# Kernel optimization log

Measured on AMD Instinct MI355X. Metric: run time of the kernel, lower is better.

Reference implementation:

```python
import jax, jax.numpy as jnp
import numpy as np

STU_NUM, ITEM_NUM, CONC_NUM, EMB_DIM, BATCH = 20000, 8000, 128, 32, 128


def setup_inputs() -> dict:
    key = jax.random.key(0)
    ks = jax.random.split(key, 12)
    # 1-based student ids, as in the original (forward does stu - 1)
    stu_list = jax.random.randint(ks[0], (BATCH,), 1, STU_NUM + 1, dtype=jnp.int32)
    stu_emb = jax.random.normal(ks[1], (STU_NUM, EMB_DIM), jnp.float32)
    item_emb = jax.random.normal(ks[2], (ITEM_NUM, EMB_DIM), jnp.float32)
    disc = jax.random.normal(ks[3], (ITEM_NUM, 1), jnp.float32)
    # binary Q-matrix (item x concept), float as in Q.float()
    Q = (jax.random.uniform(ks[4], (ITEM_NUM, CONC_NUM)) < 0.3).astype(jnp.float32)
    # emb2conc: Linear(emb_dim, conc_num) + sigmoid
    w1 = jax.random.normal(ks[5], (CONC_NUM, EMB_DIM), jnp.float32) / np.sqrt(EMB_DIM)
    b1 = jax.random.normal(ks[6], (CONC_NUM,), jnp.float32) * 0.1
    # pred_layer: Linear(conc_num, 1) + sigmoid
    wp = jax.random.normal(ks[7], (1, CONC_NUM), jnp.float32) / np.sqrt(CONC_NUM)
    bp = jax.random.normal(ks[8], (1,), jnp.float32) * 0.1
    gw_stu = jax.random.normal(ks[9], (STU_NUM, 1), jnp.float32)
    gw_Q = jax.random.normal(ks[10], (CONC_NUM, 1), jnp.float32)
    # guess_adju_layer2: Linear(1,1) + sigmoid
    w2 = jax.random.normal(ks[11], (1, 1), jnp.float32)
    b2 = jnp.zeros((1,), jnp.float32)
    return {"stu_list": stu_list, "stu_emb": stu_emb, "item_emb": item_emb,
            "disc": disc, "Q": Q, "w1": w1, "b1": b1, "wp": wp, "bp": bp,
            "gw_stu": gw_stu, "gw_Q": gw_Q, "w2": w2, "b2": b2}


def reference(stu_list, stu_emb, item_emb, disc, Q, w1, b1, wp, bp, gw_stu, gw_Q, w2, b2):
    idx = stu_list - 1                                        # 1-based -> 0-based
    stu_conc = jax.nn.sigmoid(stu_emb[idx] @ w1.T + b1)       # [B, C]
    item_conc = jax.nn.sigmoid(item_emb @ w1.T + b1)          # [I, C]
    # X = Q * (stu_emb_conc - item_emb_conc) * disc, batched over students
    X = Q[None, :, :] * (stu_conc[:, None, :] - item_conc[None, :, :]) * disc[None, :, :]  # [B, I, C]
    P = jax.nn.sigmoid(jnp.einsum('bic,c->bi', X, wp[0]) + bp[0])   # [B, I]
    Q_adju = (Q @ gw_Q)[:, 0]                                 # [I]
    g1 = jax.nn.sigmoid(gw_stu[idx] + Q_adju[None, :])        # [B,1]+[1,I] -> [B, I]
    g2 = jax.nn.sigmoid(g1 * w2[0, 0] + b2[0])                # Linear(1,1)+sigmoid
    return g2 + (1.0 - g2) * P                                # [B, I]
```

## Files before the change

### kernel.cpp

```cpp
#include <hip/hip_runtime.h>
#include <hip/hip_bf16.h>

#define STU  20000
#define ITEM 8000
#define CONC 128
#define EMB  32
#define BATCH 128

typedef short s16x8 __attribute__((ext_vector_type(8)));
typedef float f32x4 __attribute__((ext_vector_type(4)));

__device__ __forceinline__ float sigmoidf(float x) { return 1.f / (1.f + __expf(-x)); }

__global__ __launch_bounds__(256) void stu_kernel(
    const int* __restrict__ stu_list, const float* __restrict__ stu_emb,
    const float* __restrict__ w1, const float* __restrict__ b1,
    const float* __restrict__ gw_stu,
    __hip_bfloat16* __restrict__ scb_out,
    float* __restrict__ gs_out)
{
    int tid = blockIdx.x * 256 + threadIdx.x;
    int b = tid >> 7, c = tid & 127;
    int sid = stu_list[b] - 1;
    float d = b1[c];
    const float4* wrow = (const float4*)(w1 + c * EMB);
    const float4* erow = (const float4*)(stu_emb + (size_t)sid * EMB);
#pragma unroll
    for (int e4 = 0; e4 < EMB / 4; ++e4) {
        float4 w = wrow[e4], em = erow[e4];
        d += w.x * em.x + w.y * em.y + w.z * em.z + w.w * em.w;
    }
    scb_out[tid] = __float2bfloat16(sigmoidf(d) - 0.5f);
    if (c == 0) gs_out[b] = gw_stu[sid];
}

__global__ __launch_bounds__(256) void item_kernel(
    const float* __restrict__ item_emb, const float* __restrict__ Q,
    const float* __restrict__ w1, const float* __restrict__ b1,
    const float* __restrict__ wp, const float* __restrict__ gw_Q,
    __hip_bfloat16* __restrict__ qwb_out,
    float* __restrict__ t2_out,
    float* __restrict__ qa_out)
{
    const int wave = (blockIdx.x * 256 + threadIdx.x) >> 6;
    const int lane = threadIdx.x & 63;
    const int c0 = lane, c1 = lane + 64;

    float4 wa[8], wb[8];
    const float4* w0p = (const float4*)(w1 + c0 * EMB);
    const float4* w1p = (const float4*)(w1 + c1 * EMB);
#pragma unroll
    for (int j = 0; j < 8; ++j) { wa[j] = w0p[j]; wb[j] = w1p[j]; }
    const float b10 = b1[c0], b11 = b1[c1];
    const float wp0 = wp[c0], wp1 = wp[c1];
    const float gq0 = gw_Q[c0], gq1 = gw_Q[c1];

    for (int n = 0; n < 8; ++n) {
        const int i = wave * 8 + n;
        const float4* ep = (const float4*)(item_emb + (size_t)i * EMB);
        float d0 = b10, d1 = b11;
#pragma unroll
        for (int j = 0; j < 8; ++j) {
            float4 e = ep[j];
            d0 += wa[j].x * e.x + wa[j].y * e.y + wa[j].z * e.z + wa[j].w * e.w;
            d1 += wb[j].x * e.x + wb[j].y * e.y + wb[j].z * e.z + wb[j].w * e.w;
        }
        float ic0 = sigmoidf(d0), ic1 = sigmoidf(d1);
        float q0 = Q[(size_t)i * CONC + c0], q1 = Q[(size_t)i * CONC + c1];
        float u0 = q0 * wp0, u1 = q1 * wp1;
        qwb_out[(size_t)i * CONC + c0] = __float2bfloat16(u0);
        qwb_out[(size_t)i * CONC + c1] = __float2bfloat16(u1);
        float at = u0 * ic0 + u1 * ic1;
        float as = u0 + u1;
        float aq = q0 * gq0 + q1 * gq1;
#pragma unroll
        for (int off = 32; off; off >>= 1) {
            at += __shfl_xor(at, off);
            as += __shfl_xor(as, off);
            aq += __shfl_xor(aq, off);
        }
        if (lane == 0) { t2_out[i] = at - 0.5f * as; qa_out[i] = aq; }
    }
}

__global__ __launch_bounds__(256) void out_mfma(
    const __hip_bfloat16* __restrict__ qwb, const __hip_bfloat16* __restrict__ scb,
    const float* __restrict__ disc, const float* __restrict__ t2,
    const float* __restrict__ qa, const float* __restrict__ gs,
    const float* __restrict__ w2, const float* __restrict__ b2,
    const float* __restrict__ bpp,
    float* __restrict__ out)
{
    const int wid  = (blockIdx.x * 256 + threadIdx.x) >> 6;
    const int lane = threadIdx.x & 63;
    const int it = wid % 500, bt = wid / 500;
    const int i0 = it * 16, b0 = bt * 16;
    const int l15 = lane & 15, lk = lane >> 4;

    const s16x8* ap  = (const s16x8*)((const short*)scb + (b0 + l15) * CONC + lk * 8);
    const s16x8* bp8 = (const s16x8*)((const short*)qwb + (size_t)(i0 + l15) * CONC + lk * 8);

    f32x4 acc = {0.f, 0.f, 0.f, 0.f};
#pragma unroll
    for (int ks = 0; ks < 4; ++ks)
        acc = __builtin_amdgcn_mfma_f32_16x16x32_bf16(ap[ks * 4], bp8[ks * 4], acc, 0, 0, 0);

    const int i = i0 + l15;
    const float di = disc[i], ti = t2[i], qi = qa[i];
    const float W2 = w2[0], B2 = b2[0], BP = bpp[0];
#pragma unroll
    for (int r = 0; r < 4; ++r) {
        const int b = b0 + lk * 4 + r;
        float P  = sigmoidf(di * (acc[r] - ti) + BP);
        float g1 = sigmoidf(gs[b] + qi);
        float g2 = sigmoidf(fmaf(g1, W2, B2));
        out[(size_t)b * ITEM + i] = g2 + (1.f - g2) * P;
    }
}

extern "C" void kernel_launch(void* const* d_in, const int* in_sizes, int n_in,
                              void* d_out, int out_size, void* d_ws, size_t ws_size,
                              hipStream_t stream) {
    const int*   stu_list = (const int*)d_in[0];
    const float* stu_emb  = (const float*)d_in[1];
    const float* item_emb = (const float*)d_in[2];
    const float* disc     = (const float*)d_in[3];
    const float* Q        = (const float*)d_in[4];
    const float* w1       = (const float*)d_in[5];
    const float* b1       = (const float*)d_in[6];
    const float* wp       = (const float*)d_in[7];
    const float* bp       = (const float*)d_in[8];
    const float* gw_stu   = (const float*)d_in[9];
    const float* gw_Q     = (const float*)d_in[10];
    const float* w2       = (const float*)d_in[11];
    const float* b2       = (const float*)d_in[12];
    float* out = (float*)d_out;

    char* ws = (char*)d_ws;
    __hip_bfloat16* scb = (__hip_bfloat16*)ws;
    float* gs  = (float*)(ws + 32768);
    float* t2  = gs + BATCH;
    float* qa  = t2 + ITEM;
    __hip_bfloat16* qwb = (__hip_bfloat16*)(ws + 32768 + 4 * (BATCH + 2 * ITEM));

    stu_kernel<<<64, 256, 0, stream>>>(stu_list, stu_emb, w1, b1, gw_stu, scb, gs);
    item_kernel<<<250, 256, 0, stream>>>(item_emb, Q, w1, b1, wp, gw_Q, qwb, t2, qa);
    out_mfma<<<1000, 256, 0, stream>>>(qwb, scb, disc, t2, qa, gs, w2, b2, bp, out);
}
```

Before: 103.9 us.

## Fuse student, item and output stages into one MFMA kernel with LDS staging

Merges the three separate kernels into one, where each block recomputes the student concept matrix via bf16 MFMA in LDS, computes its 16 items' concept terms, and performs the output MFMA directly from shared memory. This removes two kernel launches and global workspace round trips. It adds redundant per-block student-projection work, higher LDS use that limits occupancy, and bf16 rounding of the embedding projections.

```diff
diff --git a/kernel.cpp b/kernel.cpp
--- a/kernel.cpp
+++ b/kernel.cpp
@@ -1,120 +1,157 @@
 #include <hip/hip_runtime.h>
 #include <hip/hip_bf16.h>
 
-#define STU  20000
 #define ITEM 8000
 #define CONC 128
 #define EMB  32
 #define BATCH 128
+#define NBLK 500
+#define IB   16
+#define SE_S 56
+#define SC_S 136
 
 typedef short s16x8 __attribute__((ext_vector_type(8)));
 typedef float f32x4 __attribute__((ext_vector_type(4)));
 
 __device__ __forceinline__ float sigmoidf(float x) { return 1.f / (1.f + __expf(-x)); }
-
-__global__ __launch_bounds__(256) void stu_kernel(
-    const int* __restrict__ stu_list, const float* __restrict__ stu_emb,
-    const float* __restrict__ w1, const float* __restrict__ b1,
-    const float* __restrict__ gw_stu,
-    __hip_bfloat16* __restrict__ scb_out,
-    float* __restrict__ gs_out)
-{
-    int tid = blockIdx.x * 256 + threadIdx.x;
-    int b = tid >> 7, c = tid & 127;
-    int sid = stu_list[b] - 1;
-    float d = b1[c];
-    const float4* wrow = (const float4*)(w1 + c * EMB);
-    const float4* erow = (const float4*)(stu_emb + (size_t)sid * EMB);
-#pragma unroll
-    for (int e4 = 0; e4 < EMB / 4; ++e4) {
-        float4 w = wrow[e4], em = erow[e4];
-        d += w.x * em.x + w.y * em.y + w.z * em.z + w.w * em.w;
-    }
-    scb_out[tid] = __float2bfloat16(sigmoidf(d) - 0.5f);
-    if (c == 0) gs_out[b] = gw_stu[sid];
+__device__ __forceinline__ short f2bf(float x) {
+    __hip_bfloat16 h = __float2bfloat16(x);
+    return *reinterpret_cast<short*>(&h);
+}
+__device__ __forceinline__ void cvt16(const float4* __restrict__ src, short* dst) {
+    float4 f0 = src[0], f1 = src[1], f2 = src[2], f3 = src[3];
+    s16x8 a, b;
+    a[0]=f2bf(f0.x); a[1]=f2bf(f0.y); a[2]=f2bf(f0.z); a[3]=f2bf(f0.w);
+    a[4]=f2bf(f1.x); a[5]=f2bf(f1.y); a[6]=f2bf(f1.z); a[7]=f2bf(f1.w);
+    b[0]=f2bf(f2.x); b[1]=f2bf(f2.y); b[2]=f2bf(f2.z); b[3]=f2bf(f2.w);
+    b[4]=f2bf(f3.x); b[5]=f2bf(f3.y); b[6]=f2bf(f3.z); b[7]=f2bf(f3.w);
+    *(s16x8*)dst = a;
+    *(s16x8*)(dst + 8) = b;
 }
 
-__global__ __launch_bounds__(256) void item_kernel(
-    const float* __restrict__ item_emb, const float* __restrict__ Q,
-    const float* __restrict__ w1, const float* __restrict__ b1,
-    const float* __restrict__ wp, const float* __restrict__ gw_Q,
-    __hip_bfloat16* __restrict__ qwb_out,
-    float* __restrict__ t2_out,
-    float* __restrict__ qa_out)
+__global__ __launch_bounds__(256) void fused_kernel(
+    const int* __restrict__ stu_list, const float* __restrict__ stu_emb,
+    const float* __restrict__ item_emb, const float* __restrict__ disc,
+    const float* __restrict__ Q, const float* __restrict__ w1,
+    const float* __restrict__ b1, const float* __restrict__ wp,
+    const float* __restrict__ bp_, const float* __restrict__ gw_stu,
+    const float* __restrict__ gw_Q, const float* __restrict__ w2,
+    const float* __restrict__ b2, float* __restrict__ out)
 {
-    const int wave = (blockIdx.x * 256 + threadIdx.x) >> 6;
-    const int lane = threadIdx.x & 63;
-    const int c0 = lane, c1 = lane + 64;
+    __shared__ __align__(16) short sembL[BATCH * SE_S];
+    __shared__ __align__(16) short w1L  [CONC * SE_S];
+    __shared__ __align__(16) short itembL[IB * SE_S];
+    __shared__ __align__(16) short scbL [BATCH * SC_S];
+    __shared__ __align__(16) short qwL  [IB * SC_S];
+    __shared__ float ptT[4][IB], ptQ[4][IB], gsL[BATCH];
 
-    float4 wa[8], wb[8];
-    const float4* w0p = (const float4*)(w1 + c0 * EMB);
-    const float4* w1p = (const float4*)(w1 + c1 * EMB);
-#pragma unroll
-    for (int j = 0; j < 8; ++j) { wa[j] = w0p[j]; wb[j] = w1p[j]; }
-    const float b10 = b1[c0], b11 = b1[c1];
-    const float wp0 = wp[c0], wp1 = wp[c1];
-    const float gq0 = gw_Q[c0], gq1 = gw_Q[c1];
-
-    for (int n = 0; n < 8; ++n) {
-        const int i = wave * 8 + n;
-        const float4* ep = (const float4*)(item_emb + (size_t)i * EMB);
-        float d0 = b10, d1 = b11;
-#pragma unroll
-        for (int j = 0; j < 8; ++j) {
-            float4 e = ep[j];
-            d0 += wa[j].x * e.x + wa[j].y * e.y + wa[j].z * e.z + wa[j].w * e.w;
-            d1 += wb[j].x * e.x + wb[j].y * e.y + wb[j].z * e.z + wb[j].w * e.w;
-        }
-        float ic0 = sigmoidf(d0), ic1 = sigmoidf(d1);
-        float q0 = Q[(size_t)i * CONC + c0], q1 = Q[(size_t)i * CONC + c1];
-        float u0 = q0 * wp0, u1 = q1 * wp1;
-        qwb_out[(size_t)i * CONC + c0] = __float2bfloat16(u0);
-        qwb_out[(size_t)i * CONC + c1] = __float2bfloat16(u1);
-        float at = u0 * ic0 + u1 * ic1;
-        float as = u0 + u1;
-        float aq = q0 * gq0 + q1 * gq1;
-#pragma unroll
-        for (int off = 32; off; off >>= 1) {
-            at += __shfl_xor(at, off);
-            as += __shfl_xor(as, off);
-            aq += __shfl_xor(aq, off);
-        }
-        if (lane == 0) { t2_out[i] = at - 0.5f * as; qa_out[i] = aq; }
-    }
-}
-
-__global__ __launch_bounds__(256) void out_mfma(
-    const __hip_bfloat16* __restrict__ qwb, const __hip_bfloat16* __restrict__ scb,
-    const float* __restrict__ disc, const float* __restrict__ t2,
-    const float* __restrict__ qa, const float* __restrict__ gs,
-    const float* __restrict__ w2, const float* __restrict__ b2,
-    const float* __restrict__ bpp,
-    float* __restrict__ out)
-{
-    const int wid  = (blockIdx.x * 256 + threadIdx.x) >> 6;
-    const int lane = threadIdx.x & 63;
-    const int it = wid % 500, bt = wid / 500;
-    const int i0 = it * 16, b0 = bt * 16;
+    const int tid = threadIdx.x;
+    const int i0  = blockIdx.x * IB;
+    const int w   = tid >> 6;
+    const int lane = tid & 63;
     const int l15 = lane & 15, lk = lane >> 4;
 
-    const s16x8* ap  = (const s16x8*)((const short*)scb + (b0 + l15) * CONC + lk * 8);
-    const s16x8* bp8 = (const s16x8*)((const short*)qwb + (size_t)(i0 + l15) * CONC + lk * 8);
+    {
+        int row = tid >> 1, half = tid & 1;
+        int sid = stu_list[row] - 1;
+        cvt16((const float4*)(stu_emb + (size_t)sid * EMB + half * 16),
+              &sembL[row * SE_S + half * 16]);
+        cvt16((const float4*)(w1 + row * EMB + half * 16),
+              &w1L[row * SE_S + half * 16]);
+        if (tid < 2 * IB) {
+            int ir = tid >> 1, ih = tid & 1;
+            cvt16((const float4*)(item_emb + (size_t)(i0 + ir) * EMB + ih * 16),
+                  &itembL[ir * SE_S + ih * 16]);
+        }
+        if (tid < BATCH) gsL[tid] = gw_stu[stu_list[tid] - 1];
+    }
+    __syncthreads();
 
-    f32x4 acc = {0.f, 0.f, 0.f, 0.f};
+    {
+        s16x8 af0 = *(const s16x8*)&sembL[((2 * w + 0) * 16 + l15) * SE_S + lk * 8];
+        s16x8 af1 = *(const s16x8*)&sembL[((2 * w + 1) * 16 + l15) * SE_S + lk * 8];
 #pragma unroll
-    for (int ks = 0; ks < 4; ++ks)
-        acc = __builtin_amdgcn_mfma_f32_16x16x32_bf16(ap[ks * 4], bp8[ks * 4], acc, 0, 0, 0);
+        for (int ct = 0; ct < 8; ++ct) {
+            s16x8 bf = *(const s16x8*)&w1L[(ct * 16 + l15) * SE_S + lk * 8];
+            int c = ct * 16 + l15;
+            float bc = b1[c];
+            f32x4 z = {0.f, 0.f, 0.f, 0.f};
+            f32x4 d0 = __builtin_amdgcn_mfma_f32_16x16x32_bf16(af0, bf, z, 0, 0, 0);
+            f32x4 d1 = __builtin_amdgcn_mfma_f32_16x16x32_bf16(af1, bf, z, 0, 0, 0);
+#pragma unroll
+            for (int r = 0; r < 4; ++r) {
+                scbL[((2 * w + 0) * 16 + lk * 4 + r) * SC_S + c] = f2bf(sigmoidf(d0[r] + bc) - 0.5f);
+                scbL[((2 * w + 1) * 16 + lk * 4 + r) * SC_S + c] = f2bf(sigmoidf(d1[r] + bc) - 0.5f);
+            }
+        }
+    }
 
-    const int i = i0 + l15;
-    const float di = disc[i], ti = t2[i], qi = qa[i];
-    const float W2 = w2[0], B2 = b2[0], BP = bpp[0];
+    {
+        s16x8 iaf = *(const s16x8*)&itembL[l15 * SE_S + lk * 8];
+        float at[4] = {0.f, 0.f, 0.f, 0.f}, aq[4] = {0.f, 0.f, 0.f, 0.f};
 #pragma unroll
-    for (int r = 0; r < 4; ++r) {
-        const int b = b0 + lk * 4 + r;
-        float P  = sigmoidf(di * (acc[r] - ti) + BP);
-        float g1 = sigmoidf(gs[b] + qi);
-        float g2 = sigmoidf(fmaf(g1, W2, B2));
-        out[(size_t)b * ITEM + i] = g2 + (1.f - g2) * P;
+        for (int j = 0; j < 2; ++j) {
+            int ct = 2 * w + j;
+            int c  = ct * 16 + l15;
+            s16x8 bf = *(const s16x8*)&w1L[(ct * 16 + l15) * SE_S + lk * 8];
+            f32x4 z = {0.f, 0.f, 0.f, 0.f};
+            f32x4 d = __builtin_amdgcn_mfma_f32_16x16x32_bf16(iaf, bf, z, 0, 0, 0);
+            float bc = b1[c], wpc = wp[c], gqc = gw_Q[c];
+#pragma unroll
+            for (int r = 0; r < 4; ++r) {
+                int it = lk * 4 + r;
+                float ic = sigmoidf(d[r] + bc);
+                float q  = Q[(size_t)(i0 + it) * CONC + c];
+                float u  = q * wpc;
+                qwL[it * SC_S + c] = f2bf(u);
+                at[r] += u * (ic - 0.5f);
+                aq[r] += q * gqc;
+            }
+        }
+#pragma unroll
+        for (int off = 1; off < 16; off <<= 1) {
+#pragma unroll
+            for (int r = 0; r < 4; ++r) {
+                at[r] += __shfl_xor(at[r], off);
+                aq[r] += __shfl_xor(aq[r], off);
+            }
+        }
+        if (l15 == 0) {
+#pragma unroll
+            for (int r = 0; r < 4; ++r) { ptT[w][lk * 4 + r] = at[r]; ptQ[w][lk * 4 + r] = aq[r]; }
+        }
+    }
+    __syncthreads();
+
+    {
+        s16x8 bfr[4];
+#pragma unroll
+        for (int ks = 0; ks < 4; ++ks)
+            bfr[ks] = *(const s16x8*)&qwL[l15 * SC_S + ks * 32 + lk * 8];
+
+        const int i = i0 + l15;
+        const float di = disc[i];
+        const float ti = ptT[0][l15] + ptT[1][l15] + ptT[2][l15] + ptT[3][l15];
+        const float qi = ptQ[0][l15] + ptQ[1][l15] + ptQ[2][l15] + ptQ[3][l15];
+        const float W2 = w2[0], B2 = b2[0], BP = bp_[0];
+#pragma unroll
+        for (int j = 0; j < 2; ++j) {
+            const int bt = 2 * w + j;
+            f32x4 acc = {0.f, 0.f, 0.f, 0.f};
+#pragma unroll
+            for (int ks = 0; ks < 4; ++ks) {
+                s16x8 af = *(const s16x8*)&scbL[(bt * 16 + l15) * SC_S + ks * 32 + lk * 8];
+                acc = __builtin_amdgcn_mfma_f32_16x16x32_bf16(af, bfr[ks], acc, 0, 0, 0);
+            }
+#pragma unroll
+            for (int r = 0; r < 4; ++r) {
+                int b = bt * 16 + lk * 4 + r;
+                float P  = sigmoidf(di * (acc[r] - ti) + BP);
+                float g1 = sigmoidf(gsL[b] + qi);
+                float g2 = sigmoidf(fmaf(g1, W2, B2));
+                out[(size_t)b * ITEM + i] = g2 + (1.f - g2) * P;
+            }
+        }
     }
 }
 
@@ -136,14 +173,6 @@
     const float* b2       = (const float*)d_in[12];
     float* out = (float*)d_out;
 
-    char* ws = (char*)d_ws;
-    __hip_bfloat16* scb = (__hip_bfloat16*)ws;
-    float* gs  = (float*)(ws + 32768);
-    float* t2  = gs + BATCH;
-    float* qa  = t2 + ITEM;
-    __hip_bfloat16* qwb = (__hip_bfloat16*)(ws + 32768 + 4 * (BATCH + 2 * ITEM));
-
-    stu_kernel<<<64, 256, 0, stream>>>(stu_list, stu_emb, w1, b1, gw_stu, scb, gs);
-    item_kernel<<<250, 256, 0, stream>>>(item_emb, Q, w1, b1, wp, gw_Q, qwb, t2, qa);
-    out_mfma<<<1000, 256, 0, stream>>>(qwb, scb, disc, t2, qa, gs, w2, b2, bp, out);
+    fused_kernel<<<NBLK, 256, 0, stream>>>(stu_list, stu_emb, item_emb, disc, Q,
+                                           w1, b1, wp, bp, gw_stu, gw_Q, w2, b2, out);
 }
```

Result: faster. 92.20 us (-11.2%).
